# Kernel optimization log

Hardware: AMD Instinct MI355X
Metric: run time of the kernel (lower is better)

## Reference

```python
import jax, jax.numpy as jnp
import numpy as np

N_NODES = 1000000
N_EDGES = 2000000
N_FEAT = 11          # QM9 num_features
HIDDEN = 64
N_CLASSES = 19       # QM9 num_classes
BATCH = 128


def setup_inputs() -> dict:
    key = jax.random.key(0)
    k = jax.random.split(key, 8)
    x = jax.random.normal(k[0], (N_NODES, N_FEAT), dtype=jnp.float32)
    edge_index = jax.random.randint(k[1], (2, N_EDGES), 0, N_NODES, dtype=jnp.int64)
    y = jax.random.normal(k[2], (BATCH, N_CLASSES), dtype=jnp.float32)
    batch = jnp.sort(jax.random.randint(k[3], (N_NODES,), 0, BATCH, dtype=jnp.int64))
    # GCNConv params: weight [in, hidden], bias [hidden]
    W_conv = jax.random.normal(k[4], (N_FEAT, HIDDEN), dtype=jnp.float32) / np.sqrt(N_FEAT)
    b_conv = jnp.zeros((HIDDEN,), dtype=jnp.float32)
    # Final linear: [hidden, classes]
    W_lin = jax.random.normal(k[5], (HIDDEN, N_CLASSES), dtype=jnp.float32) / np.sqrt(HIDDEN)
    b_lin = jnp.zeros((N_CLASSES,), dtype=jnp.float32)
    return {"x": x, "edge_index": edge_index, "y": y, "batch": batch,
            "W_conv": W_conv, "b_conv": b_conv, "W_lin": W_lin, "b_lin": b_lin}


def reference(x, edge_index, y, batch, W_conv, b_conv, W_lin, b_lin):
    row, col = edge_index[0], edge_index[1]  # source -> target
    # GCN symmetric normalization (add_self_loops=False): deg over targets
    ones = jnp.ones((edge_index.shape[1],), dtype=x.dtype)
    deg = jax.ops.segment_sum(ones, col, num_segments=N_NODES)
    dinv = jnp.where(deg > 0, jax.lax.rsqrt(jnp.maximum(deg, 1.0)), 0.0)
    norm = dinv[row] * dinv[col]  # [E]
    # Transform then aggregate: gather at source, scatter-add at target
    xw = x @ W_conv                                    # [N, H]
    msgs = xw[row] * norm[:, None]                     # [E, H]
    agg = jax.ops.segment_sum(msgs, col, num_segments=N_NODES) + b_conv
    h = jax.nn.relu(agg)                               # [N, H]
    # global_mean_pool over batch ids (size=BATCH)
    summed = jax.ops.segment_sum(h, batch, num_segments=BATCH)   # [B, H]
    counts = jax.ops.segment_sum(jnp.ones((N_NODES,), dtype=x.dtype), batch, num_segments=BATCH)
    pooled = summed / jnp.maximum(counts, 1.0)[:, None]
    # dropout p=0.5 is identity in eval mode
    return pooled @ W_lin + b_lin                      # [B, classes]
```

## Files before the change

kernel.cpp:

```cpp
#include <hip/hip_runtime.h>

#define N_NODES   1000000
#define N_EDGES   2000000
#define N_FEAT    11
#define HIDDEN    64
#define BATCH     128
#define N_CLASSES 19

#define NPB     1024
#define NBUCK   977
#define BCAP    2560
#define EPB     4096
#define PBLK    489
#define NSLOT   8
#define NCHUNK  (NBUCK * 4)

__device__ __forceinline__ unsigned f2b(float v) {
    unsigned u = __float_as_uint(v);
    return (u + 0x7FFFu + ((u >> 16) & 1u)) >> 16;
}

__global__ __launch_bounds__(256) void part_kernel(const int* __restrict__ row,
                                                   const int* __restrict__ col,
                                                   int* __restrict__ bcnt,
                                                   int* __restrict__ part) {
    __shared__ int lh[NPB];
    const int t = threadIdx.x;
    for (int i = t; i < NPB; i += 256) lh[i] = 0;
    __syncthreads();
    const int base = blockIdx.x * EPB;
#pragma unroll
    for (int i = 0; i < EPB / 256; ++i) {
        int e = base + i * 256 + t;
        if (e < N_EDGES) atomicAdd(&lh[col[e] >> 10], 1);
    }
    __syncthreads();
    for (int b = t; b < NBUCK; b += 256) {
        int v = lh[b];
        if (v) lh[b] = b * BCAP + atomicAdd(&bcnt[b], v);
    }
    __syncthreads();
#pragma unroll
    for (int i = 0; i < EPB / 256; ++i) {
        int e = base + i * 256 + t;
        if (e < N_EDGES) {
            int c = col[e];
            int pos = atomicAdd(&lh[c >> 10], 1);
            part[pos] = (row[e] << 10) | (c & (NPB - 1));
        }
    }
}

__global__ __launch_bounds__(256) void sort2_kernel(const int* __restrict__ part,
                                                    const int* __restrict__ bcnt,
                                                    const float* __restrict__ x,
                                                    int* __restrict__ srcs,
                                                    int* __restrict__ cstart5,
                                                    int* __restrict__ nstart,
                                                    unsigned short* __restrict__ ndeg,
                                                    float* __restrict__ dinv,
                                                    unsigned short* __restrict__ xs) {
    __shared__ int cnt[NPB];
    __shared__ int off[NPB];
    __shared__ int tsum[256];
    const int t = threadIdx.x, b = blockIdx.x;
    for (int i = t; i < NPB; i += 256) cnt[i] = 0;
    __syncthreads();
    const int s0 = b * BCAP, e0 = s0 + bcnt[b];
    for (int j = s0 + t; j < e0; j += 256)
        atomicAdd(&cnt[part[j] & (NPB - 1)], 1);
    __syncthreads();
    const int i0 = t * 4;
    int c0 = cnt[i0], c1 = cnt[i0 + 1], c2 = cnt[i0 + 2], c3 = cnt[i0 + 3];
    int s = c0 + c1 + c2 + c3;
    tsum[t] = s;
    __syncthreads();
    for (int o = 1; o < 256; o <<= 1) {
        int a = (t >= o) ? tsum[t - o] : 0;
        __syncthreads();
        tsum[t] += a;
        __syncthreads();
    }
    int ex = tsum[t] - s;
    off[i0] = ex; off[i0 + 1] = ex + c0; off[i0 + 2] = ex + c0 + c1; off[i0 + 3] = ex + c0 + c1 + c2;
    __syncthreads();
    if (t < 4) cstart5[b * 5 + t] = s0 + off[t * 256];
    if (t == 4) cstart5[b * 5 + 4] = e0;
    for (int i = t; i < NPB; i += 256) {
        int n = b * NPB + i;
        if (n < N_NODES) {
            int d = cnt[i];
            float dv = d ? rsqrtf((float)d) : 0.0f;
            dinv[n]   = dv;
            ndeg[n]   = (unsigned short)d;
            nstart[n] = s0 + off[i];
            const float* xr = x + (size_t)n * N_FEAT;
            unsigned h[11];
#pragma unroll
            for (int k = 0; k < 11; ++k) h[k] = f2b(dv * xr[k]);
            uint4 A, B;
            A.x = h[0] | (h[1] << 16); A.y = h[2] | (h[3] << 16);
            A.z = h[4] | (h[5] << 16); A.w = h[6] | (h[7] << 16);
            B.x = h[8] | (h[9] << 16); B.y = h[10]; B.z = 0u; B.w = 0u;
            uint4* o = (uint4*)(xs + (size_t)n * 16);
            o[0] = A; o[1] = B;
        }
    }
    __syncthreads();
    for (int j = s0 + t; j < e0; j += 256) {
        int p  = part[j];
        int cl = p & (NPB - 1);
        int pos = s0 + atomicAdd(&off[cl], 1);
        srcs[pos] = p >> 10;
    }
}

__global__ __launch_bounds__(256) void gather_pool_kernel(
    const int* __restrict__ cstart5, const int* __restrict__ srcs,
    const unsigned short* __restrict__ xs, const int* __restrict__ nstart,
    const unsigned short* __restrict__ ndeg, const float* __restrict__ dinv,
    const int* __restrict__ batch, const float* __restrict__ Wc,
    const float* __restrict__ bc, float* __restrict__ pooled,
    float* __restrict__ countsf) {
    __shared__ float facc[256 * 12];
    __shared__ int   sj0[256];
    __shared__ int   sdeg[256];
    __shared__ float sdinv[256];
    __shared__ int   sbid[256];
    __shared__ int   sperm[256];
    __shared__ int   dcnt[32];
    __shared__ int   doff[32];
    __shared__ float pbuf[NSLOT * HIDDEN];
    __shared__ int   pcnt[NSLOT];
    const int t = threadIdx.x, lane = t & 63, w = t >> 6;
    const int base = blockIdx.x * 256;
    {
        int n = base + t;
        bool v = n < N_NODES;
        sj0[t]   = v ? nstart[n] : 0;
        sdeg[t]  = v ? (int)ndeg[n] : 0;
        sdinv[t] = v ? dinv[n] : 0.0f;
        sbid[t]  = v ? batch[n] : -1;
    }
    for (int i = t; i < NSLOT * HIDDEN; i += 256) pbuf[i] = 0.0f;
    if (t < NSLOT) pcnt[t] = 0;
    if (t < 32)    dcnt[t] = 0;
    __syncthreads();
    int mybin = sdeg[t] < 31 ? sdeg[t] : 31;
    atomicAdd(&dcnt[mybin], 1);
    __syncthreads();
    if (t < 32) {
        int r = 0;
        for (int i = 0; i < t; ++i) r += dcnt[i];
        doff[t] = r;
    }
    __syncthreads();
    int pos = atomicAdd(&doff[mybin], 1);
    sperm[pos] = t;
    __syncthreads();

    {
        int i  = sperm[t];
        int j0 = sj0[i], d = sdeg[i];
        float acc[11];
#pragma unroll
        for (int k = 0; k < 11; ++k) acc[k] = 0.0f;
        for (int j = j0; j < j0 + d; ++j) {
            int r = srcs[j];
            const uint4* xr = (const uint4*)(xs + (size_t)r * 16);
            uint4 A = xr[0];
            uint2 B = *(const uint2*)(xr + 1);
            acc[0]  += __uint_as_float(A.x << 16);
            acc[1]  += __uint_as_float(A.x & 0xFFFF0000u);
            acc[2]  += __uint_as_float(A.y << 16);
            acc[3]  += __uint_as_float(A.y & 0xFFFF0000u);
            acc[4]  += __uint_as_float(A.z << 16);
            acc[5]  += __uint_as_float(A.z & 0xFFFF0000u);
            acc[6]  += __uint_as_float(A.w << 16);
            acc[7]  += __uint_as_float(A.w & 0xFFFF0000u);
            acc[8]  += __uint_as_float(B.x << 16);
            acc[9]  += __uint_as_float(B.x & 0xFFFF0000u);
            acc[10] += __uint_as_float(B.y << 16);
        }
        float* f = &facc[i * 12];
#pragma unroll
        for (int k = 0; k < 11; ++k) f[k] = acc[k];
    }
    __syncthreads();

    float wk[N_FEAT];
#pragma unroll
    for (int k = 0; k < N_FEAT; ++k) wk[k] = Wc[k * HIDDEN + lane];
    const float bias = bc[lane];
    const int bid0 = sbid[0];
    int cur = -1; float accp = 0.0f; int cntp = 0;
    for (int i = w * 64; i < w * 64 + 64; ++i) {
        int bid = sbid[i];
        if (bid < 0) break;
        if (bid != cur) {
            if (cur >= 0) {
                int slot = cur - bid0;
                if (slot >= 0 && slot < NSLOT) {
                    atomicAdd(&pbuf[slot * HIDDEN + lane], accp);
                    if (lane == 0) atomicAdd(&pcnt[slot], cntp);
                } else {
                    atomicAdd(&pooled[(size_t)cur * HIDDEN + lane], accp);
                    if (lane == 0) atomicAdd(&countsf[cur], (float)cntp);
                }
            }
            cur = bid; accp = 0.0f; cntp = 0;
        }
        float s = 0.0f;
#pragma unroll
        for (int k = 0; k < N_FEAT; ++k)
            s = fmaf(wk[k], facc[i * 12 + k], s);
        accp += fmaxf(fmaf(sdinv[i], s, bias), 0.0f);
        ++cntp;
    }
    if (cur >= 0) {
        int slot = cur - bid0;
        if (slot >= 0 && slot < NSLOT) {
            atomicAdd(&pbuf[slot * HIDDEN + lane], accp);
            if (lane == 0) atomicAdd(&pcnt[slot], cntp);
        } else {
            atomicAdd(&pooled[(size_t)cur * HIDDEN + lane], accp);
            if (lane == 0) atomicAdd(&countsf[cur], (float)cntp);
        }
    }
    __syncthreads();
    for (int s = w; s < NSLOT; s += 4) {
        int c = pcnt[s];
        if (c > 0) {
            atomicAdd(&pooled[(size_t)(bid0 + s) * HIDDEN + lane], pbuf[s * HIDDEN + lane]);
            if (lane == 0) atomicAdd(&countsf[bid0 + s], (float)c);
        }
    }
}

__global__ void final_kernel(const float* __restrict__ pooled, const float* __restrict__ counts,
                             const float* __restrict__ Wl, const float* __restrict__ bl,
                             float* __restrict__ out) {
    int i = blockIdx.x * blockDim.x + threadIdx.x;
    if (i >= BATCH * N_CLASSES) return;
    int b = i / N_CLASSES;
    int c = i - b * N_CLASSES;
    float inv = 1.0f / fmaxf(counts[b], 1.0f);
    float s = bl[c];
#pragma unroll 8
    for (int h = 0; h < HIDDEN; ++h)
        s = fmaf(pooled[b * HIDDEN + h] * inv, Wl[h * N_CLASSES + c], s);
    out[i] = s;
}

extern "C" void kernel_launch(void* const* d_in, const int* in_sizes, int n_in,
                              void* d_out, int out_size, void* d_ws, size_t ws_size,
                              hipStream_t stream) {
    const float* x     = (const float*)d_in[0];
    const int*   ei    = (const int*)d_in[1];
    const int*   batch = (const int*)d_in[3];
    const float* Wc    = (const float*)d_in[4];
    const float* bc    = (const float*)d_in[5];
    const float* Wl    = (const float*)d_in[6];
    const float* bl    = (const float*)d_in[7];
    float*       out   = (float*)d_out;

    int*            bcnt    = (int*)d_ws;
    float*          pooled  = (float*)(bcnt + 1024);
    float*          countsf = pooled + BATCH * HIDDEN;
    int*            cstart5 = (int*)(countsf + BATCH);
    unsigned short* xs      = (unsigned short*)(cstart5 + 4896);
    int*            nstart  = (int*)(xs + (size_t)N_NODES * 16);
    unsigned short* ndeg    = (unsigned short*)(nstart + N_NODES);
    float*          dinv    = (float*)(ndeg + N_NODES);
    int*            part    = (int*)(dinv + N_NODES);
    int*            srcs    = part + (size_t)NBUCK * BCAP;

    size_t zero_bytes = (1024 + BATCH * HIDDEN + BATCH) * 4;
    hipMemsetAsync(d_ws, 0, zero_bytes, stream);

    const int* row = ei;
    const int* col = ei + N_EDGES;

    part_kernel <<<PBLK, 256, 0, stream>>>(row, col, bcnt, part);
    sort2_kernel<<<NBUCK, 256, 0, stream>>>(part, bcnt, x, srcs, cstart5, nstart, ndeg, dinv, xs);
    gather_pool_kernel<<<NCHUNK, 256, 0, stream>>>(cstart5, srcs, xs, nstart, ndeg, dinv,
                                                   batch, Wc, bc, pooled, countsf);
    final_kernel<<<(BATCH * N_CLASSES + 255) / 256, 256, 0, stream>>>(pooled, countsf, Wl, bl, out);
}
```

Before: 249.5 us.

## Double partition bucket size, vectorize edge reads, pad shared feature stride

Buckets now cover 2048 nodes each, so there are half as many partition and sort blocks, each handling twice the edges. The partition kernel reads row and col as int4 to cut load instructions. The unused cstart5 output is dropped and the gather kernel's shared accumulator stride goes from 12 to 13 to reduce LDS bank conflicts. Fewer, larger blocks reduce per-block overhead but lower occupancy and parallelism in the sort stage, and packed row indices must now fit in 21 bits.

```diff
diff --git a/kernel.cpp b/kernel.cpp
--- a/kernel.cpp
+++ b/kernel.cpp
@@ -7,13 +7,14 @@
 #define BATCH     128
 #define N_CLASSES 19
 
-#define NPB     1024
-#define NBUCK   977
-#define BCAP    2560
-#define EPB     4096
-#define PBLK    489
+#define NPB     2048
+#define NBUCK   489
+#define BCAP    5120
+#define EPB     8192
+#define PBLK    245
 #define NSLOT   8
-#define NCHUNK  (NBUCK * 4)
+#define NCHUNK  3907
+#define FSTR    13
 
 __device__ __forceinline__ unsigned f2b(float v) {
     unsigned u = __float_as_uint(v);
@@ -24,15 +25,21 @@
                                                    const int* __restrict__ col,
                                                    int* __restrict__ bcnt,
                                                    int* __restrict__ part) {
-    __shared__ int lh[NPB];
+    __shared__ int lh[512];
     const int t = threadIdx.x;
-    for (int i = t; i < NPB; i += 256) lh[i] = 0;
-    __syncthreads();
-    const int base = blockIdx.x * EPB;
-#pragma unroll
-    for (int i = 0; i < EPB / 256; ++i) {
-        int e = base + i * 256 + t;
-        if (e < N_EDGES) atomicAdd(&lh[col[e] >> 10], 1);
+    for (int i = t; i < 512; i += 256) lh[i] = 0;
+    __syncthreads();
+    const int q0 = (blockIdx.x * EPB) >> 2;
+    const int4* col4 = (const int4*)col;
+    const int4* row4 = (const int4*)row;
+#pragma unroll
+    for (int i = 0; i < EPB / 1024; ++i) {
+        int q = q0 + i * 256 + t;
+        if (q < N_EDGES / 4) {
+            int4 c = col4[q];
+            atomicAdd(&lh[c.x >> 11], 1); atomicAdd(&lh[c.y >> 11], 1);
+            atomicAdd(&lh[c.z >> 11], 1); atomicAdd(&lh[c.w >> 11], 1);
+        }
     }
     __syncthreads();
     for (int b = t; b < NBUCK; b += 256) {
@@ -41,12 +48,16 @@
     }
     __syncthreads();
 #pragma unroll
-    for (int i = 0; i < EPB / 256; ++i) {
-        int e = base + i * 256 + t;
-        if (e < N_EDGES) {
-            int c = col[e];
-            int pos = atomicAdd(&lh[c >> 10], 1);
-            part[pos] = (row[e] << 10) | (c & (NPB - 1));
+    for (int i = 0; i < EPB / 1024; ++i) {
+        int q = q0 + i * 256 + t;
+        if (q < N_EDGES / 4) {
+            int4 c = col4[q];
+            int4 r = row4[q];
+            int p;
+            p = atomicAdd(&lh[c.x >> 11], 1); part[p] = (r.x << 11) | (c.x & (NPB - 1));
+            p = atomicAdd(&lh[c.y >> 11], 1); part[p] = (r.y << 11) | (c.y & (NPB - 1));
+            p = atomicAdd(&lh[c.z >> 11], 1); part[p] = (r.z << 11) | (c.z & (NPB - 1));
+            p = atomicAdd(&lh[c.w >> 11], 1); part[p] = (r.w << 11) | (c.w & (NPB - 1));
         }
     }
 }
@@ -55,7 +66,6 @@
                                                     const int* __restrict__ bcnt,
                                                     const float* __restrict__ x,
                                                     int* __restrict__ srcs,
-                                                    int* __restrict__ cstart5,
                                                     int* __restrict__ nstart,
                                                     unsigned short* __restrict__ ndeg,
                                                     float* __restrict__ dinv,
@@ -70,9 +80,10 @@
     for (int j = s0 + t; j < e0; j += 256)
         atomicAdd(&cnt[part[j] & (NPB - 1)], 1);
     __syncthreads();
-    const int i0 = t * 4;
-    int c0 = cnt[i0], c1 = cnt[i0 + 1], c2 = cnt[i0 + 2], c3 = cnt[i0 + 3];
-    int s = c0 + c1 + c2 + c3;
+    const int i0 = t * 8;
+    int c[8], s = 0;
+#pragma unroll
+    for (int q = 0; q < 8; ++q) { c[q] = cnt[i0 + q]; s += c[q]; }
     tsum[t] = s;
     __syncthreads();
     for (int o = 1; o < 256; o <<= 1) {
@@ -81,11 +92,10 @@
         tsum[t] += a;
         __syncthreads();
     }
-    int ex = tsum[t] - s;
-    off[i0] = ex; off[i0 + 1] = ex + c0; off[i0 + 2] = ex + c0 + c1; off[i0 + 3] = ex + c0 + c1 + c2;
-    __syncthreads();
-    if (t < 4) cstart5[b * 5 + t] = s0 + off[t * 256];
-    if (t == 4) cstart5[b * 5 + 4] = e0;
+    int run = tsum[t] - s;
+#pragma unroll
+    for (int q = 0; q < 8; ++q) { off[i0 + q] = run; run += c[q]; }
+    __syncthreads();
     for (int i = t; i < NPB; i += 256) {
         int n = b * NPB + i;
         if (n < N_NODES) {
@@ -111,18 +121,17 @@
         int p  = part[j];
         int cl = p & (NPB - 1);
         int pos = s0 + atomicAdd(&off[cl], 1);
-        srcs[pos] = p >> 10;
+        srcs[pos] = p >> 11;
     }
 }
 
 __global__ __launch_bounds__(256) void gather_pool_kernel(
-    const int* __restrict__ cstart5, const int* __restrict__ srcs,
-    const unsigned short* __restrict__ xs, const int* __restrict__ nstart,
-    const unsigned short* __restrict__ ndeg, const float* __restrict__ dinv,
-    const int* __restrict__ batch, const float* __restrict__ Wc,
-    const float* __restrict__ bc, float* __restrict__ pooled,
-    float* __restrict__ countsf) {
-    __shared__ float facc[256 * 12];
+    const int* __restrict__ srcs, const unsigned short* __restrict__ xs,
+    const int* __restrict__ nstart, const unsigned short* __restrict__ ndeg,
+    const float* __restrict__ dinv, const int* __restrict__ batch,
+    const float* __restrict__ Wc, const float* __restrict__ bc,
+    float* __restrict__ pooled, float* __restrict__ countsf) {
+    __shared__ float facc[256 * FSTR];
     __shared__ int   sj0[256];
     __shared__ int   sdeg[256];
     __shared__ float sdinv[256];
@@ -182,7 +191,7 @@
             acc[9]  += __uint_as_float(B.x & 0xFFFF0000u);
             acc[10] += __uint_as_float(B.y << 16);
         }
-        float* f = &facc[i * 12];
+        float* f = &facc[i * FSTR];
 #pragma unroll
         for (int k = 0; k < 11; ++k) f[k] = acc[k];
     }
@@ -213,7 +222,7 @@
         float s = 0.0f;
 #pragma unroll
         for (int k = 0; k < N_FEAT; ++k)
-            s = fmaf(wk[k], facc[i * 12 + k], s);
+            s = fmaf(wk[k], facc[i * FSTR + k], s);
         accp += fmaxf(fmaf(sdinv[i], s, bias), 0.0f);
         ++cntp;
     }
@@ -265,25 +274,24 @@
     float*       out   = (float*)d_out;
 
     int*            bcnt    = (int*)d_ws;
-    float*          pooled  = (float*)(bcnt + 1024);
+    float*          pooled  = (float*)(bcnt + 512);
     float*          countsf = pooled + BATCH * HIDDEN;
-    int*            cstart5 = (int*)(countsf + BATCH);
-    unsigned short* xs      = (unsigned short*)(cstart5 + 4896);
+    unsigned short* xs      = (unsigned short*)(countsf + BATCH);
     int*            nstart  = (int*)(xs + (size_t)N_NODES * 16);
     unsigned short* ndeg    = (unsigned short*)(nstart + N_NODES);
     float*          dinv    = (float*)(ndeg + N_NODES);
     int*            part    = (int*)(dinv + N_NODES);
     int*            srcs    = part + (size_t)NBUCK * BCAP;
 
-    size_t zero_bytes = (1024 + BATCH * HIDDEN + BATCH) * 4;
+    size_t zero_bytes = (512 + BATCH * HIDDEN + BATCH) * 4;
     hipMemsetAsync(d_ws, 0, zero_bytes, stream);
 
     const int* row = ei;
     const int* col = ei + N_EDGES;
 
     part_kernel <<<PBLK, 256, 0, stream>>>(row, col, bcnt, part);
-    sort2_kernel<<<NBUCK, 256, 0, stream>>>(part, bcnt, x, srcs, cstart5, nstart, ndeg, dinv, xs);
-    gather_pool_kernel<<<NCHUNK, 256, 0, stream>>>(cstart5, srcs, xs, nstart, ndeg, dinv,
+    sort2_kernel<<<NBUCK, 256, 0, stream>>>(part, bcnt, x, srcs, nstart, ndeg, dinv, xs);
+    gather_pool_kernel<<<NCHUNK, 256, 0, stream>>>(srcs, xs, nstart, ndeg, dinv,
                                                    batch, Wc, bc, pooled, countsf);
     final_kernel<<<(BATCH * N_CLASSES + 255) / 256, 256, 0, stream>>>(pooled, countsf, Wl, bl, out);
 }
```

Result: no change. 244.9 us (-1.9%).
